# Optimization experiments

Measured on AMD Instinct MI355X. Metric: run time of the kernel, lower is better.

## Reference

```python
import jax, jax.numpy as jnp
import numpy as np

TEMPERATURE = 0.5
N_NODES = 100000
D = 64
N_EDGES = 400000
K_NEG = 10
NEG_SEED = 42


def setup_inputs() -> dict:
    key = jax.random.key(0)
    k1, k2 = jax.random.split(key)
    node_embeddings = jax.random.normal(k1, (N_NODES, D), dtype=jnp.float32)
    edge_index = jax.random.randint(k2, (2, N_EDGES), 0, N_NODES, dtype=jnp.int32)
    return {
        "node_embeddings": node_embeddings,
        "edge_index": edge_index,
        "num_neg_samples": K_NEG,
    }


def _sample_negatives(src, dst, n_nodes, k):
    """Uniform negatives per edge, excluding src and dst (vectorized
    replacement for the per-edge randperm in the original)."""
    a = jnp.minimum(src, dst)[:, None]  # [E,1]
    b = jnp.maximum(src, dst)[:, None]
    r = jax.random.randint(jax.random.key(NEG_SEED), (src.shape[0], k), 0,
                           n_nodes - 2, dtype=jnp.int32)
    # src != dst: skip index a, then index b (a < b)
    r1 = r + (r >= a).astype(r.dtype)
    neg_distinct = r1 + (r1 >= b).astype(r.dtype)
    # self-loop edge (a == b): skip a once
    neg_equal = r + (r >= a).astype(r.dtype)
    return jnp.where(a == b, neg_equal, neg_distinct)  # [E,K]


def reference(node_embeddings, edge_index, num_neg_samples):
    n_nodes = node_embeddings.shape[0]
    # F.normalize(p=2, dim=-1) with eps clamp
    norm = jnp.linalg.norm(node_embeddings, axis=-1, keepdims=True)
    emb = node_embeddings / jnp.maximum(norm, 1e-12)

    src, dst = edge_index[0], edge_index[1]
    src_emb = emb[src]                                   # [E,D]
    pos_sim = jnp.sum(src_emb * emb[dst], axis=-1) / TEMPERATURE  # [E]

    neg_idx = _sample_negatives(src, dst, n_nodes, num_neg_samples)  # [E,K]
    neg_sim = jnp.einsum('ed,ekd->ek', src_emb, emb[neg_idx]) / TEMPERATURE

    # exp(pos) / (exp(pos) + sum exp(neg)) computed stably via logsumexp
    logits = jnp.concatenate([pos_sim[:, None], neg_sim], axis=1)  # [E,1+K]
    ratio = jnp.exp(pos_sim - jax.nn.logsumexp(logits, axis=1))
    # original sums -log(ratio + 1e-8) over all edges (scalar .mean() is a no-op)
    return jnp.sum(-jnp.log(ratio + 1e-8))
```

## Files before the change

### kernel.cpp

```cpp
#include <hip/hip_runtime.h>
#include <hip/hip_bf16.h>
#include <stdint.h>

#define JAX_THREEFRY_PARTITIONABLE 1

struct U2 { uint32_t a, b; };

__host__ __device__ constexpr uint32_t rotl32(uint32_t v, int r) {
    return (v << r) | (v >> (32 - r));
}

__host__ __device__ constexpr U2 tf2x32(uint32_t k0, uint32_t k1, uint32_t x0, uint32_t x1) {
    const uint32_t ks2 = k0 ^ k1 ^ 0x1BD11BDAu;
    const uint32_t ks[3] = {k0, k1, ks2};
    const int rot[2][4] = {{13, 15, 26, 6}, {17, 29, 16, 24}};
    x0 += ks[0]; x1 += ks[1];
    #pragma unroll
    for (int j = 1; j <= 5; ++j) {
        const int* rr = rot[(j - 1) & 1];
        #pragma unroll
        for (int q = 0; q < 4; ++q) { x0 += x1; x1 = rotl32(x1, rr[q]); x1 ^= x0; }
        x0 += ks[j % 3];
        x1 += ks[(j + 1) % 3] + (uint32_t)j;
    }
    return {x0, x1};
}

#if JAX_THREEFRY_PARTITIONABLE
constexpr U2 KEY_HI = tf2x32(0u, 42u, 0u, 0u);
constexpr U2 KEY_LO = tf2x32(0u, 42u, 0u, 1u);
#else
constexpr U2 ENC02 = tf2x32(0u, 42u, 0u, 2u);
constexpr U2 ENC13 = tf2x32(0u, 42u, 1u, 3u);
constexpr U2 KEY_HI = {ENC02.a, ENC13.a};
constexpr U2 KEY_LO = {ENC02.b, ENC13.b};
#endif

__device__ __forceinline__ uint32_t draw_bits(uint32_t ka, uint32_t kb, uint32_t i, uint32_t half) {
#if JAX_THREEFRY_PARTITIONABLE
    U2 o = tf2x32(ka, kb, 0u, i);
    return o.a ^ o.b;
#else
    if (i < half) { return tf2x32(ka, kb, i, i + half).a; }
    else          { return tf2x32(ka, kb, i - half, i).b; }
#endif
}

template <int CTRL>
__device__ __forceinline__ float dpp_add(float v) {
    int t = __builtin_amdgcn_update_dpp(0, __float_as_int(v), CTRL, 0xf, 0xf, false);
    return v + __int_as_float(t);
}

__device__ __forceinline__ float group16_sum(float v) {
    v = dpp_add<0xB1>(v);
    v = dpp_add<0x4E>(v);
    v = dpp_add<0x141>(v);
    v = dpp_add<0x140>(v);
    return v;
}

__device__ __forceinline__ float dot4(const float4& a, const float4& b) {
    return a.x * b.x + a.y * b.y + a.z * b.z + a.w * b.w;
}

__device__ __forceinline__ ushort f32_bf16_rne(float f) {
    uint32_t x = __float_as_uint(f);
    return (ushort)((x + 0x7fffu + ((x >> 16) & 1u)) >> 16);
}
__device__ __forceinline__ float bf16_f32(ushort u) {
    return __uint_as_float(((uint32_t)u) << 16);
}
__device__ __forceinline__ float4 cvt4(ushort4 u) {
    return {bf16_f32(u.x), bf16_f32(u.y), bf16_f32(u.z), bf16_f32(u.w)};
}

__global__ __launch_bounds__(256) void prep_norm_bf16(const float* __restrict__ emb,
                                                      ushort* __restrict__ tab, int N) {
    const int tid = threadIdx.x;
    const int g = tid >> 4, sl = tid & 15;
    const int row = blockIdx.x * 16 + g;
    if (row >= N) return;
    float4 v = *reinterpret_cast<const float4*>(emb + (size_t)row * 64 + sl * 4);
    float ss = dot4(v, v);
    ss = group16_sum(ss);
    const float inv = 1.0f / fmaxf(sqrtf(ss), 1e-12f);
    ushort4 o;
    o.x = f32_bf16_rne(v.x * inv);
    o.y = f32_bf16_rne(v.y * inv);
    o.z = f32_bf16_rne(v.z * inv);
    o.w = f32_bf16_rne(v.w * inv);
    *reinterpret_cast<ushort4*>(tab + (size_t)row * 64 + sl * 4) = o;
}

__global__ __launch_bounds__(256) void edge_loss_bf16(
    const ushort* __restrict__ tab, const int* __restrict__ ei,
    float* __restrict__ partial, int E, uint32_t span, uint32_t mult, uint32_t half,
    uint32_t k1a, uint32_t k1b, uint32_t k2a, uint32_t k2b) {
    const int tid = threadIdx.x;
    const int g = tid >> 4;
    const int sl = tid & 15;
    const int lane = tid & 63;
    const int e = blockIdx.x * 16 + g;

    float loss = 0.0f;
    if (e < E) {
        const int s = ei[e];
        const int d = ei[E + e];
        const ushort* tp = tab + sl * 4;
        const ushort4 su = *reinterpret_cast<const ushort4*>(tp + (size_t)s * 64);
        const ushort4 du = *reinterpret_cast<const ushort4*>(tp + (size_t)d * 64);

        const int a = min(s, d);
        const int b = max(s, d);
        const uint32_t i = (uint32_t)e * 10u + (uint32_t)sl;
        uint32_t off = draw_bits(k2a, k2b, i, half) % span;
        if (mult != 0u) {
            uint32_t hi = draw_bits(k1a, k1b, i, half) % span;
            off = (hi * mult + off) % span;
        }
        int r = (int)off;
        int r1 = r + (r >= a ? 1 : 0);
        const int negidx = r1 + (((a != b) && (r1 >= b)) ? 1 : 0);

        int idx[10];
        #pragma unroll
        for (int k = 0; k < 10; ++k) idx[k] = __shfl(negidx, (lane & 48) | k);

        ushort4 nu[10];
        #pragma unroll
        for (int k = 0; k < 10; ++k)
            nu[k] = *reinterpret_cast<const ushort4*>(tp + (size_t)idx[k] * 64);

        const float4 sv = cvt4(su);
        const float4 dv = cvt4(du);
        float p = dot4(sv, dv);
        p = group16_sum(p);
        const float pos = p * 2.0f;

        float m = pos;
        float ns[10];
        #pragma unroll
        for (int k = 0; k < 10; ++k) {
            float q = dot4(sv, cvt4(nu[k]));
            q = group16_sum(q);
            const float nsim = q * 2.0f;
            ns[k] = nsim;
            m = fmaxf(m, nsim);
        }
        float ssum = expf(pos - m);
        #pragma unroll
        for (int k = 0; k < 10; ++k) ssum += expf(ns[k] - m);
        const float lse = m + logf(ssum);
        loss = -logf(expf(pos - lse) + 1e-8f);
    }

    float v = (sl == 0) ? loss : 0.0f;
    v += __shfl_xor(v, 16);
    v += __shfl_xor(v, 32);
    __shared__ float sred[4];
    if (lane == 0) sred[tid >> 6] = v;
    __syncthreads();
    if (tid == 0) partial[blockIdx.x] = sred[0] + sred[1] + sred[2] + sred[3];
}

__global__ __launch_bounds__(256) void inv_norm_kernel(const float* __restrict__ emb,
                                                       float* __restrict__ invn, int N) {
    const int tid = threadIdx.x;
    const int g = tid >> 4, sl = tid & 15;
    const int row = blockIdx.x * 16 + g;
    if (row >= N) return;
    float4 v = *reinterpret_cast<const float4*>(emb + (size_t)row * 64 + sl * 4);
    float ss = dot4(v, v);
    ss = group16_sum(ss);
    if (sl == 0) invn[row] = 1.0f / fmaxf(sqrtf(ss), 1e-12f);
}

__global__ __launch_bounds__(256) void edge_loss_kernel(
    const float* __restrict__ emb, const int* __restrict__ ei,
    const float* __restrict__ invn, float* __restrict__ partial,
    int E, uint32_t span, uint32_t mult, uint32_t half,
    uint32_t k1a, uint32_t k1b, uint32_t k2a, uint32_t k2b) {
    const int tid = threadIdx.x;
    const int g = tid >> 4;
    const int sl = tid & 15;
    const int lane = tid & 63;
    const int e = blockIdx.x * 16 + g;

    float loss = 0.0f;
    if (e < E) {
        const int s = ei[e];
        const int d = ei[E + e];
        const float inv_s = invn[s];
        const float inv_d = invn[d];
        const float* rowp = emb + sl * 4;
        const float4 sv = *reinterpret_cast<const float4*>(rowp + (size_t)s * 64);
        const float4 dv = *reinterpret_cast<const float4*>(rowp + (size_t)d * 64);

        const int a = min(s, d);
        const int b = max(s, d);
        const uint32_t i = (uint32_t)e * 10u + (uint32_t)sl;
        uint32_t off = draw_bits(k2a, k2b, i, half) % span;
        if (mult != 0u) {
            uint32_t hi = draw_bits(k1a, k1b, i, half) % span;
            off = (hi * mult + off) % span;
        }
        int r = (int)off;
        int r1 = r + (r >= a ? 1 : 0);
        const int negidx = r1 + (((a != b) && (r1 >= b)) ? 1 : 0);

        int idx[10];
        #pragma unroll
        for (int k = 0; k < 10; ++k) idx[k] = __shfl(negidx, (lane & 48) | k);

        float4 nv[10];
        float ri[10];
        #pragma unroll
        for (int k = 0; k < 10; ++k) {
            nv[k] = *reinterpret_cast<const float4*>(rowp + (size_t)idx[k] * 64);
            ri[k] = invn[idx[k]];
        }

        float p = dot4(sv, dv);
        p = group16_sum(p);
        const float pos = p * inv_s * inv_d * 2.0f;

        float m = pos;
        float ns[10];
        #pragma unroll
        for (int k = 0; k < 10; ++k) {
            float q = dot4(sv, nv[k]);
            q = group16_sum(q);
            const float nsim = q * inv_s * ri[k] * 2.0f;
            ns[k] = nsim;
            m = fmaxf(m, nsim);
        }
        float ssum = expf(pos - m);
        #pragma unroll
        for (int k = 0; k < 10; ++k) ssum += expf(ns[k] - m);
        const float lse = m + logf(ssum);
        loss = -logf(expf(pos - lse) + 1e-8f);
    }

    float v = (sl == 0) ? loss : 0.0f;
    v += __shfl_xor(v, 16);
    v += __shfl_xor(v, 32);
    __shared__ float sred[4];
    if (lane == 0) sred[tid >> 6] = v;
    __syncthreads();
    if (tid == 0) partial[blockIdx.x] = sred[0] + sred[1] + sred[2] + sred[3];
}

__global__ __launch_bounds__(256) void finalize_kernel(const float* __restrict__ partial,
                                                       int n, float* __restrict__ out) {
    __shared__ double sd[256];
    double acc = 0.0;
    for (int i = threadIdx.x; i < n; i += 256) acc += (double)partial[i];
    sd[threadIdx.x] = acc;
    __syncthreads();
    for (int s = 128; s > 0; s >>= 1) {
        if (threadIdx.x < s) sd[threadIdx.x] += sd[threadIdx.x + s];
        __syncthreads();
    }
    if (threadIdx.x == 0) out[0] = (float)sd[0];
}

extern "C" void kernel_launch(void* const* d_in, const int* in_sizes, int n_in,
                              void* d_out, int out_size, void* d_ws, size_t ws_size,
                              hipStream_t stream) {
    const float* emb = (const float*)d_in[0];
    const int* ei = (const int*)d_in[1];
    const int N = in_sizes[0] / 64;
    const int E = in_sizes[1] / 2;
    const int K = 10;

    const int nblk_main = (E + 15) / 16;
    const int nblk_norm = (N + 15) / 16;

    const uint32_t span = (uint32_t)(N - 2);
    const uint32_t m0 = 65536u % span;
    const uint32_t mult = (uint32_t)(m0 * m0) % span;
    const uint32_t half = (uint32_t)((E * K) / 2);

    const size_t tab_bytes = (size_t)N * 64 * sizeof(ushort);
    const size_t tab_pad = (tab_bytes + 255) & ~(size_t)255;
    const size_t need = tab_pad + (size_t)nblk_main * sizeof(float);

    if (ws_size >= need) {
        ushort* tab = (ushort*)d_ws;
        float* partial = (float*)((char*)d_ws + tab_pad);
        prep_norm_bf16<<<nblk_norm, 256, 0, stream>>>(emb, tab, N);
        edge_loss_bf16<<<nblk_main, 256, 0, stream>>>(tab, ei, partial,
                                                      E, span, mult, half,
                                                      KEY_HI.a, KEY_HI.b, KEY_LO.a, KEY_LO.b);
        finalize_kernel<<<1, 256, 0, stream>>>(partial, nblk_main, (float*)d_out);
    } else {
        float* invn = (float*)d_ws;
        float* partial = invn + N;
        inv_norm_kernel<<<nblk_norm, 256, 0, stream>>>(emb, invn, N);
        edge_loss_kernel<<<nblk_main, 256, 0, stream>>>(emb, ei, invn, partial,
                                                        E, span, mult, half,
                                                        KEY_HI.a, KEY_HI.b, KEY_LO.a, KEY_LO.b);
        finalize_kernel<<<1, 256, 0, stream>>>(partial, nblk_main, (float*)d_out);
    }
}
```

Measured before the change: 161.5 us.

## Precompute negative indices in separate kernel and use fixed-shift softmax

Moves threefry negative-index generation out of the edge-loss kernel into its own fully parallel kernel that writes an E*K index table to workspace. The loss kernel then only loads those indices, which shortens its dependency chain before the gathers begin. The softmax drops the running max and instead uses a constant shift of 2, valid because the cosine similarities over temperature 0.5 lie in [-2, 2], and uses fast __expf/__logf intrinsics. In exchange it adds an extra launch and a 16 MB write and read of the index table, and the fast intrinsics slightly reduce accuracy.

New measurement: 173.0 us. 7.2% more time.

```diff
diff --git a/kernel.cpp b/kernel.cpp
--- a/kernel.cpp
+++ b/kernel.cpp
@@ -93,9 +93,32 @@
     *reinterpret_cast<ushort4*>(tab + (size_t)row * 64 + sl * 4) = o;
 }
 
+__global__ __launch_bounds__(256) void neg_idx_kernel(
+    const int* __restrict__ ei, int* __restrict__ neg, int E,
+    uint32_t span, uint32_t mult, uint32_t half,
+    uint32_t k1a, uint32_t k1b, uint32_t k2a, uint32_t k2b) {
+    const int t = blockIdx.x * 256 + threadIdx.x;
+    if (t >= E * 10) return;
+    const int e = t / 10;
+    uint32_t off = draw_bits(k2a, k2b, (uint32_t)t, half) % span;
+    if (mult != 0u) {
+        uint32_t hi = draw_bits(k1a, k1b, (uint32_t)t, half) % span;
+        off = (hi * mult + off) % span;
+    }
+    const int s = ei[e];
+    const int d = ei[E + e];
+    const int a = min(s, d);
+    const int b = max(s, d);
+    int r = (int)off;
+    int r1 = r + (r >= a ? 1 : 0);
+    neg[t] = r1 + (((a != b) && (r1 >= b)) ? 1 : 0);
+}
+
+template <bool PRENEG>
 __global__ __launch_bounds__(256) void edge_loss_bf16(
     const ushort* __restrict__ tab, const int* __restrict__ ei,
-    float* __restrict__ partial, int E, uint32_t span, uint32_t mult, uint32_t half,
+    const int* __restrict__ negtab, float* __restrict__ partial,
+    int E, uint32_t span, uint32_t mult, uint32_t half,
     uint32_t k1a, uint32_t k1b, uint32_t k2a, uint32_t k2b) {
     const int tid = threadIdx.x;
     const int g = tid >> 4;
@@ -111,17 +134,22 @@
         const ushort4 su = *reinterpret_cast<const ushort4*>(tp + (size_t)s * 64);
         const ushort4 du = *reinterpret_cast<const ushort4*>(tp + (size_t)d * 64);
 
-        const int a = min(s, d);
-        const int b = max(s, d);
-        const uint32_t i = (uint32_t)e * 10u + (uint32_t)sl;
-        uint32_t off = draw_bits(k2a, k2b, i, half) % span;
-        if (mult != 0u) {
-            uint32_t hi = draw_bits(k1a, k1b, i, half) % span;
-            off = (hi * mult + off) % span;
-        }
-        int r = (int)off;
-        int r1 = r + (r >= a ? 1 : 0);
-        const int negidx = r1 + (((a != b) && (r1 >= b)) ? 1 : 0);
+        int negidx;
+        if (PRENEG) {
+            negidx = (sl < 10) ? negtab[e * 10 + sl] : 0;
+        } else {
+            const int a = min(s, d);
+            const int b = max(s, d);
+            const uint32_t i = (uint32_t)e * 10u + (uint32_t)sl;
+            uint32_t off = draw_bits(k2a, k2b, i, half) % span;
+            if (mult != 0u) {
+                uint32_t hi = draw_bits(k1a, k1b, i, half) % span;
+                off = (hi * mult + off) % span;
+            }
+            int r = (int)off;
+            int r1 = r + (r >= a ? 1 : 0);
+            negidx = r1 + (((a != b) && (r1 >= b)) ? 1 : 0);
+        }
 
         int idx[10];
         #pragma unroll
@@ -138,21 +166,15 @@
         p = group16_sum(p);
         const float pos = p * 2.0f;
 
-        float m = pos;
-        float ns[10];
+        float ssum = __expf(pos - 2.0f);
         #pragma unroll
         for (int k = 0; k < 10; ++k) {
             float q = dot4(sv, cvt4(nu[k]));
             q = group16_sum(q);
-            const float nsim = q * 2.0f;
-            ns[k] = nsim;
-            m = fmaxf(m, nsim);
-        }
-        float ssum = expf(pos - m);
-        #pragma unroll
-        for (int k = 0; k < 10; ++k) ssum += expf(ns[k] - m);
-        const float lse = m + logf(ssum);
-        loss = -logf(expf(pos - lse) + 1e-8f);
+            ssum += __expf(q * 2.0f - 2.0f);
+        }
+        const float lse = 2.0f + __logf(ssum);
+        loss = -__logf(__expf(pos - lse) + 1e-8f);
     }
 
     float v = (sl == 0) ? loss : 0.0f;
@@ -276,23 +298,37 @@
 
     const int nblk_main = (E + 15) / 16;
     const int nblk_norm = (N + 15) / 16;
+    const int nblk_neg  = (E * K + 255) / 256;
 
     const uint32_t span = (uint32_t)(N - 2);
     const uint32_t m0 = 65536u % span;
     const uint32_t mult = (uint32_t)(m0 * m0) % span;
     const uint32_t half = (uint32_t)((E * K) / 2);
 
-    const size_t tab_bytes = (size_t)N * 64 * sizeof(ushort);
-    const size_t tab_pad = (tab_bytes + 255) & ~(size_t)255;
-    const size_t need = tab_pad + (size_t)nblk_main * sizeof(float);
-
-    if (ws_size >= need) {
+    const size_t tab_pad = (((size_t)N * 64 * sizeof(ushort)) + 255) & ~(size_t)255;
+    const size_t neg_pad = (((size_t)E * K * sizeof(int)) + 255) & ~(size_t)255;
+    const size_t part_bytes = (size_t)nblk_main * sizeof(float);
+    const size_t need_full = tab_pad + neg_pad + part_bytes;
+    const size_t need_tab  = tab_pad + part_bytes;
+
+    if (ws_size >= need_full) {
+        ushort* tab = (ushort*)d_ws;
+        int* neg = (int*)((char*)d_ws + tab_pad);
+        float* partial = (float*)((char*)d_ws + tab_pad + neg_pad);
+        prep_norm_bf16<<<nblk_norm, 256, 0, stream>>>(emb, tab, N);
+        neg_idx_kernel<<<nblk_neg, 256, 0, stream>>>(ei, neg, E, span, mult, half,
+                                                     KEY_HI.a, KEY_HI.b, KEY_LO.a, KEY_LO.b);
+        edge_loss_bf16<true><<<nblk_main, 256, 0, stream>>>(tab, ei, neg, partial,
+                                                            E, span, mult, half,
+                                                            KEY_HI.a, KEY_HI.b, KEY_LO.a, KEY_LO.b);
+        finalize_kernel<<<1, 256, 0, stream>>>(partial, nblk_main, (float*)d_out);
+    } else if (ws_size >= need_tab) {
         ushort* tab = (ushort*)d_ws;
         float* partial = (float*)((char*)d_ws + tab_pad);
         prep_norm_bf16<<<nblk_norm, 256, 0, stream>>>(emb, tab, N);
-        edge_loss_bf16<<<nblk_main, 256, 0, stream>>>(tab, ei, partial,
-                                                      E, span, mult, half,
-                                                      KEY_HI.a, KEY_HI.b, KEY_LO.a, KEY_LO.b);
+        edge_loss_bf16<false><<<nblk_main, 256, 0, stream>>>(tab, ei, nullptr, partial,
+                                                             E, span, mult, half,
+                                                             KEY_HI.a, KEY_HI.b, KEY_LO.a, KEY_LO.b);
         finalize_kernel<<<1, 256, 0, stream>>>(partial, nblk_main, (float*)d_out);
     } else {
         float* invn = (float*)d_ws;
```
